# Optimization experiments

Measured on AMD Instinct MI355X. Metric: run time of the kernel, lower is better.

The kernel has to match this reference:

```python
import jax, jax.numpy as jnp
import numpy as np

N = 50000
E = 800000
IN_FEAT = 256
HIDDEN = 256
NUM_CLASS = 10
NUM_GRAPHS = 512
LAYERS = 2


def setup_inputs() -> dict:
    key = jax.random.key(0)
    ks = jax.random.split(key, 10)
    x = jax.random.normal(ks[0], (N, IN_FEAT), dtype=jnp.float32)
    edge_index = jax.random.randint(ks[1], (2, E), 0, N, dtype=jnp.int32)
    batch = jnp.sort(jax.random.randint(ks[2], (N,), 0, NUM_GRAPHS, dtype=jnp.int32))
    s_in = 1.0 / np.sqrt(IN_FEAT)
    s_h = 1.0 / np.sqrt(HIDDEN)
    enc_W = jax.random.uniform(ks[3], (IN_FEAT, HIDDEN), jnp.float32, -s_in, s_in)
    enc_b = jax.random.uniform(ks[4], (HIDDEN,), jnp.float32, -s_in, s_in)
    conv_W = jax.random.uniform(ks[5], (LAYERS, HIDDEN, HIDDEN), jnp.float32, -s_h, s_h)
    conv_b = jax.random.uniform(ks[6], (LAYERS, HIDDEN), jnp.float32, -s_h, s_h)
    out_W = jax.random.uniform(ks[7], (HIDDEN, NUM_CLASS), jnp.float32, -s_h, s_h)
    out_b = jax.random.uniform(ks[8], (NUM_CLASS,), jnp.float32, -s_h, s_h)
    return {"x": x, "edge_index": edge_index, "batch": batch,
            "enc_W": enc_W, "enc_b": enc_b,
            "conv_W": conv_W, "conv_b": conv_b,
            "out_W": out_W, "out_b": out_b}


def _gcn_conv(x, row, col, deg_norm_edge, W, b):
    # PyG GCNConv: linear transform, then normalized scatter-add aggregation.
    h = x @ W                                   # [N, H]
    msg = h[row] * deg_norm_edge[:, None]       # [E+N, H] gather + scale
    out = jax.ops.segment_sum(msg, col, num_segments=N)  # scatter-add
    return out + b


def reference(x, edge_index, batch, enc_W, enc_b, conv_W, conv_b, out_W, out_b):
    # self-loops appended once (same structure every layer)
    loops = jnp.arange(N, dtype=edge_index.dtype)
    row = jnp.concatenate([edge_index[0], loops])  # source
    col = jnp.concatenate([edge_index[1], loops])  # target
    deg = jax.ops.segment_sum(jnp.ones_like(col, dtype=x.dtype), col, num_segments=N)
    dinv = jnp.where(deg > 0, jax.lax.rsqrt(deg), 0.0)
    norm = dinv[row] * dinv[col]                # symmetric GCN normalization per edge

    h = x @ enc_W + enc_b
    for i in range(LAYERS):
        h = jax.nn.relu(_gcn_conv(h, row, col, norm, conv_W[i], conv_b[i]))

    # global_mean_pool over `batch` segment ids
    sums = jax.ops.segment_sum(h, batch, num_segments=NUM_GRAPHS)
    cnts = jax.ops.segment_sum(jnp.ones((N,), dtype=h.dtype), batch, num_segments=NUM_GRAPHS)
    pooled = sums / jnp.maximum(cnts, 1.0)[:, None]

    # dropout is identity in eval mode
    return pooled @ out_W + out_b
```

## Files before the change

kernel.cpp:

```cpp
#include <hip/hip_runtime.h>

#define NN 50000
#define NE 800000
#define HD 256
#define NG 512
#define NC 10
#define GEMM_G ((NN + 31) / 32)
#define NP 196
#define HB 200
#define CHUNK (NE / HB)
#define NODES_PER_HB (NN / HB)

typedef unsigned short u16;
typedef unsigned char u8;
typedef short v8s __attribute__((ext_vector_type(8)));
typedef float v4f __attribute__((ext_vector_type(4)));
typedef float v2f __attribute__((ext_vector_type(2)));
typedef u16 v4u __attribute__((ext_vector_type(4)));
typedef u16 v8u __attribute__((ext_vector_type(8)));

static __device__ __forceinline__ float bf2f(u16 u) {
    return __uint_as_float(((unsigned)u) << 16);
}
static __device__ __forceinline__ u16 f2bf(float f) {
    unsigned u = __float_as_uint(f);
    unsigned r = (u + 0x7fffu + ((u >> 16) & 1u)) >> 16;
    return (u16)r;
}
static __device__ __forceinline__ int clampi(int v, int lo, int hi) {
    return min(max(v, lo), hi);
}
static __device__ __forceinline__ float ldf(const void* p, size_t i, int isbf) {
    return isbf ? bf2f(((const u16*)p)[i]) : ((const float*)p)[i];
}

static __device__ __forceinline__ u8 f32_to_fp8(float f) {
#if __has_builtin(__builtin_amdgcn_cvt_pk_fp8_f32)
    int r = __builtin_amdgcn_cvt_pk_fp8_f32(f, f, 0, false);
    return (u8)(r & 0xff);
#else
    float a = fabsf(f);
    unsigned s = (__float_as_uint(f) >> 31) << 7;
    if (a < 0.0009765625f) return (u8)s;
    a = fminf(a, 448.f);
    if (a < 0.015625f) {
        int m = (int)(a * 512.f + 0.5f);
        return (u8)(s | min(m, 7));
    }
    unsigned u = __float_as_uint(a);
    unsigned r = u + 0x0007FFFFu + ((u >> 20) & 1u);
    int e = (int)(r >> 23) - 127 + 7;
    if (e > 15) return (u8)(s | 0x7E);
    unsigned m = (r >> 20) & 7u;
    return (u8)(s | ((unsigned)e << 3) | m);
#endif
}
static __device__ __forceinline__ v4f fp8x4_to_f32(unsigned v) {
#if __has_builtin(__builtin_amdgcn_cvt_pk_f32_fp8)
    v2f lo = __builtin_amdgcn_cvt_pk_f32_fp8(v, false);
    v2f hi = __builtin_amdgcn_cvt_pk_f32_fp8(v, true);
    return (v4f){lo[0], lo[1], hi[0], hi[1]};
#else
    v4f o;
#pragma unroll
    for (int j = 0; j < 4; j++) {
        unsigned b = (v >> (8 * j)) & 0xffu;
        unsigned e = (b >> 3) & 15u, m = b & 7u;
        float val = e ? __uint_as_float(((e + 120u) << 23) | (m << 20))
                      : (float)m * 0.001953125f;
        o[j] = (b & 0x80u) ? -val : val;
    }
    return o;
#endif
}

__global__ void k_detect(const u16* __restrict__ xu, int* __restrict__ mode) {
    __shared__ int cnt;
    if (threadIdx.x == 0) cnt = 0;
    __syncthreads();
    int bad = 0;
    for (int i = threadIdx.x; i < 4096; i += 256) {
        float v = bf2f(xu[2 * i]);
        float av = fabsf(v);
        if (av > 100.f || (av < 1e-3f && av != 0.f)) bad++;
    }
    atomicAdd(&cnt, bad);
    __syncthreads();
    if (threadIdx.x == 0) mode[0] = (cnt > 1024) ? 0 : 1;
}

__global__ void k_prep(const void* __restrict__ enc_W, const void* __restrict__ conv_W,
                       const void* __restrict__ enc_b, const void* __restrict__ conv_b,
                       const void* __restrict__ out_b,
                       u16* __restrict__ Wp, float* __restrict__ biasf,
                       const int* __restrict__ modep) {
    int md = modep[0];
    int b = blockIdx.x;
    if (b < 768) {
        int wi = b >> 8;
        int n = b & 255, k = threadIdx.x;
        const void* W = (wi == 0) ? enc_W : conv_W;
        size_t off = (wi == 0) ? 0 : (size_t)(wi - 1) * HD * HD;
        int nt = n >> 4, m = n & 15;
        int ks = k >> 5, q = (k >> 3) & 3, j = k & 7;
        size_t idx = ((((size_t)nt * 8 + ks) * 64) + q * 16 + m) * 8 + j;
        Wp[(size_t)wi * HD * HD + idx] = f2bf(ldf(W, off + (size_t)k * HD + n, md));
    } else {
        for (int j = threadIdx.x; j < 768 + NC; j += 256) {
            float v = (j < 256) ? ldf(enc_b, j, md)
                    : (j < 768) ? ldf(conv_b, j - 256, md)
                                : ldf(out_b, j - 768, md);
            biasf[j] = v;
        }
    }
}

static __device__ __forceinline__ void hist_body(
        int b, const int* __restrict__ ecol, const int* __restrict__ batch,
        int* __restrict__ bh, int* __restrict__ gptr, int* hist) {
    int tid = threadIdx.x;
    if (tid < NP) hist[tid] = 0;
    __syncthreads();
    int e0 = b * CHUNK;
    for (int i = tid; i < CHUNK; i += 256) {
        int c = clampi(ecol[e0 + i], 0, NN - 1);
        atomicAdd(&hist[c >> 8], 1);
    }
    int n0 = b * NODES_PER_HB;
    for (int i = tid; i < NODES_PER_HB; i += 256) {
        int idx = n0 + i;
        int bb = clampi(batch[idx], 0, NG - 1);
        int bp = (idx == 0) ? -1 : clampi(batch[idx - 1], 0, NG - 1);
        for (int g = bp + 1; g <= bb; g++) gptr[g] = idx;
        if (idx == NN - 1)
            for (int g = bb + 1; g <= NG; g++) gptr[g] = NN;
    }
    __syncthreads();
    if (tid < NP) bh[(size_t)tid * HB + b] = hist[tid];
}

static __device__ __forceinline__ void scat_body(
        int b, const int* __restrict__ erow, const int* __restrict__ ecol,
        const int* __restrict__ pptr, const int* __restrict__ base,
        unsigned* __restrict__ pairbuf, int* lfill) {
    int tid = threadIdx.x;
    if (tid < NP) lfill[tid] = 0;
    __syncthreads();
    int e0 = b * CHUNK;
    for (int i = tid; i < CHUNK; i += 256) {
        int c = clampi(ecol[e0 + i], 0, NN - 1);
        int rw = clampi(erow[e0 + i], 0, NN - 1);
        int p = c >> 8;
        int r = atomicAdd(&lfill[p], 1);
        int pos = pptr[p] + base[(size_t)p * HB + b] + r;
        pairbuf[pos] = ((unsigned)rw << 8) | (unsigned)(c & 255);
    }
}

static __device__ __forceinline__ void gemm_body(
        int bid, u16* As, const void* __restrict__ A, const u16* __restrict__ Wp,
        const float* __restrict__ biasf, void* __restrict__ out,
        int M, int hasBias, int outFp8, int amode) {
    int tid = threadIdx.x;
    int wave = tid >> 6;
    int lane = tid & 63;
    int row0 = bid * 32;
    if (row0 >= M) return;
    int m = lane & 15, q = lane >> 4;

#pragma unroll
    for (int it = 0; it < 4; it++) {
        int fb = it * 4 + wave;
        int mt = fb >> 3, ks = fb & 7;
        int row = min(row0 + mt * 16 + m, M - 1);
        int colE = ks * 32 + q * 8;
        v8s v;
        if (amode) {
            v = *(const v8s*)((const u16*)A + (size_t)row * HD + colE);
        } else {
            const float* af = (const float*)A + (size_t)row * HD + colE;
            v4f x0 = *(const v4f*)af;
            v4f x1 = *(const v4f*)(af + 4);
            v[0] = (short)f2bf(x0[0]); v[1] = (short)f2bf(x0[1]);
            v[2] = (short)f2bf(x0[2]); v[3] = (short)f2bf(x0[3]);
            v[4] = (short)f2bf(x1[0]); v[5] = (short)f2bf(x1[1]);
            v[6] = (short)f2bf(x1[2]); v[7] = (short)f2bf(x1[3]);
        }
        *(v8s*)&As[((size_t)fb * 64 + lane) * 8] = v;
    }
    __syncthreads();

    v4f acc[2][4];
#pragma unroll
    for (int i = 0; i < 2; i++)
#pragma unroll
        for (int j = 0; j < 4; j++) acc[i][j] = (v4f){0.f, 0.f, 0.f, 0.f};

    const u16* wp = Wp + (size_t)wave * 4 * 8 * 64 * 8;

#pragma unroll
    for (int ks = 0; ks < 8; ks++) {
        v8s bfr[4];
#pragma unroll
        for (int nt = 0; nt < 4; nt++)
            bfr[nt] = *(const v8s*)(wp + ((size_t)(nt * 8 + ks) * 64 + lane) * 8);
        v8s a[2];
#pragma unroll
        for (int mt = 0; mt < 2; mt++)
            a[mt] = *(const v8s*)&As[((size_t)(mt * 8 + ks) * 64 + lane) * 8];
#pragma unroll
        for (int mt = 0; mt < 2; mt++)
#pragma unroll
            for (int nt = 0; nt < 4; nt++)
                acc[mt][nt] = __builtin_amdgcn_mfma_f32_16x16x32_bf16(
                    a[mt], bfr[nt], acc[mt][nt], 0, 0, 0);
    }
    if (outFp8) {
#pragma unroll
        for (int mt = 0; mt < 2; mt++) {
#pragma unroll
            for (int nt = 0; nt < 4; nt++) {
                int ocol = wave * 64 + nt * 16 + m;
#pragma unroll
                for (int r = 0; r < 4; r++) {
                    int orow = row0 + mt * 16 + q * 4 + r;
                    if (orow < M)
                        ((u8*)out)[(size_t)orow * HD + ocol] =
                            f32_to_fp8(acc[mt][nt][r] * 32.f);
                }
            }
        }
    } else {
#pragma unroll
        for (int mt = 0; mt < 2; mt++) {
#pragma unroll
            for (int nt = 0; nt < 4; nt++) {
                int ocol = wave * 64 + nt * 16 + m;
                float badd = hasBias ? biasf[ocol] : 0.f;
#pragma unroll
                for (int r = 0; r < 4; r++) {
                    int orow = row0 + mt * 16 + q * 4 + r;
                    if (orow < M)
                        ((u16*)out)[(size_t)orow * HD + ocol] =
                            f2bf(acc[mt][nt][r] + badd);
                }
            }
        }
    }
}

static __device__ __forceinline__ void agg_node(
        const u8* __restrict__ t, const int* __restrict__ cptr,
        const int* __restrict__ csrc, const float* __restrict__ dinv,
        const float* __restrict__ biasf, int node, int lane, float* o) {
    int half = lane >> 5;
    int f0 = (lane & 31) * 8;
    const u8* tf = t + f0;
    float dn = dinv[node];
    float a[8];
#pragma unroll
    for (int k = 0; k < 8; k++) a[k] = 0.f;

    if (half == 0) {
        uint2 sv = *(const uint2*)(tf + (size_t)node * HD);
        v4f lo = fp8x4_to_f32(sv.x), hi = fp8x4_to_f32(sv.y);
#pragma unroll
        for (int k = 0; k < 4; k++) {
            a[k] += lo[k] * dn;
            a[k + 4] += hi[k] * dn;
        }
    }

    int e0 = cptr[node], e1 = cptr[node + 1];
    e1 = clampi(e1, 0, NE);
    e0 = clampi(e0, 0, e1);
    int e = e0;
    for (; e + 16 <= e1; e += 16) {
        int s[8];
#pragma unroll
        for (int j = 0; j < 8; j++)
            s[j] = clampi(csrc[e + 2 * j + half], 0, NN - 1);
        uint2 rv[8];
        float wv[8];
#pragma unroll
        for (int j = 0; j < 8; j++) {
            rv[j] = *(const uint2*)(tf + (size_t)s[j] * HD);
            wv[j] = dinv[s[j]];
        }
#pragma unroll
        for (int j = 0; j < 8; j++) {
            v4f lo = fp8x4_to_f32(rv[j].x), hi = fp8x4_to_f32(rv[j].y);
#pragma unroll
            for (int k = 0; k < 4; k++) {
                a[k] = fmaf(lo[k], wv[j], a[k]);
                a[k + 4] = fmaf(hi[k], wv[j], a[k + 4]);
            }
        }
    }
    for (; e + 2 <= e1; e += 2) {
        int s = clampi(csrc[e + half], 0, NN - 1);
        uint2 rv = *(const uint2*)(tf + (size_t)s * HD);
        float wv = dinv[s];
        v4f lo = fp8x4_to_f32(rv.x), hi = fp8x4_to_f32(rv.y);
#pragma unroll
        for (int k = 0; k < 4; k++) {
            a[k] = fmaf(lo[k], wv, a[k]);
            a[k + 4] = fmaf(hi[k], wv, a[k + 4]);
        }
    }
    if (e < e1 && half == 0) {
        int s = clampi(csrc[e], 0, NN - 1);
        uint2 rv = *(const uint2*)(tf + (size_t)s * HD);
        float wv = dinv[s];
        v4f lo = fp8x4_to_f32(rv.x), hi = fp8x4_to_f32(rv.y);
#pragma unroll
        for (int k = 0; k < 4; k++) {
            a[k] = fmaf(lo[k], wv, a[k]);
            a[k + 4] = fmaf(hi[k], wv, a[k + 4]);
        }
    }
#pragma unroll
    for (int k = 0; k < 8; k++) a[k] += __shfl_xor(a[k], 32, 64);

    float sc = dn * 0.03125f;
    v4f b0 = *(const v4f*)(biasf + f0);
    v4f b1 = *(const v4f*)(biasf + f0 + 4);
#pragma unroll
    for (int k = 0; k < 4; k++) {
        o[k] = fmaxf(fmaf(a[k], sc, b0[k]), 0.f);
        o[k + 4] = fmaxf(fmaf(a[k + 4], sc, b1[k]), 0.f);
    }
}

__global__ __launch_bounds__(256) void k_gemm(
        const void* __restrict__ A, const u16* __restrict__ Wp,
        const float* __restrict__ biasf, void* __restrict__ out,
        int M, int hasBias, int outFp8,
        const int* __restrict__ modep, int forceBf) {
    __shared__ u16 As[16 * 64 * 8];
    gemm_body(blockIdx.x, As, A, Wp, biasf, out, M, hasBias, outFp8,
              forceBf ? 1 : modep[0]);
}

__global__ __launch_bounds__(256) void k_hist(
        const int* __restrict__ ecol, const int* __restrict__ batch,
        int* __restrict__ bh, int* __restrict__ gptr) {
    __shared__ int hist[NP];
    hist_body(blockIdx.x, ecol, batch, bh, gptr, hist);
}

__global__ __launch_bounds__(256) void k_scat(
        const int* __restrict__ erow, const int* __restrict__ ecol,
        const int* __restrict__ pptr, const int* __restrict__ base,
        unsigned* __restrict__ pairbuf) {
    __shared__ int lfill[NP];
    scat_body(blockIdx.x, erow, ecol, pptr, base, pairbuf, lfill);
}

__global__ __launch_bounds__(256) void k_gemm_hist(
        const void* __restrict__ A, const u16* __restrict__ Wp,
        const float* __restrict__ biasf, void* __restrict__ out,
        int M, int hasBias, const int* __restrict__ modep, int forceBf,
        const int* __restrict__ ecol, const int* __restrict__ batch,
        int* __restrict__ bh, int* __restrict__ gptr) {
    __shared__ u16 As[16 * 64 * 8];
    __shared__ int hist[NP];
    if (blockIdx.x < HB) {
        hist_body(blockIdx.x, ecol, batch, bh, gptr, hist);
    } else {
        gemm_body(blockIdx.x - HB, As, A, Wp, biasf, out, M, hasBias, 0,
                  forceBf ? 1 : modep[0]);
    }
}

__global__ __launch_bounds__(256) void k_scat_gemm1(
        const void* __restrict__ A, const u16* __restrict__ Wp,
        void* __restrict__ out, int M,
        const int* __restrict__ erow, const int* __restrict__ ecol,
        const int* __restrict__ pptr, const int* __restrict__ base,
        unsigned* __restrict__ pairbuf) {
    __shared__ u16 As[16 * 64 * 8];
    __shared__ int lfill[NP];
    if (blockIdx.x < HB) {
        scat_body(blockIdx.x, erow, ecol, pptr, base, pairbuf, lfill);
    } else {
        gemm_body(blockIdx.x - HB, As, A, Wp, nullptr, out, M, 0, 1, 1);
    }
}

__global__ __launch_bounds__(256) void k_aggregate2(
        const u8* __restrict__ t, const int* __restrict__ cptr,
        const int* __restrict__ csrc, const float* __restrict__ dinv,
        const float* __restrict__ biasf, u16* __restrict__ out) {
    int wave = threadIdx.x >> 6, lane = threadIdx.x & 63;
    int node = blockIdx.x * 4 + wave;
    if (node >= NN) return;
    float o[8];
    agg_node(t, cptr, csrc, dinv, biasf, node, lane, o);
    if (lane < 32) {
        v8u pk;
#pragma unroll
        for (int k = 0; k < 8; k++) pk[k] = f2bf(o[k]);
        *(v8u*)(out + (size_t)node * HD + lane * 8) = pk;
    }
}

__global__ __launch_bounds__(256) void k_scanA(
        const int* __restrict__ bh, int* __restrict__ base, int* __restrict__ ptot) {
    int p = blockIdx.x, t = threadIdx.x;
    int v = (t < HB) ? bh[(size_t)p * HB + t] : 0;
    __shared__ int sh[256];
    sh[t] = v;
    __syncthreads();
    for (int off = 1; off < 256; off <<= 1) {
        int x = (t >= off) ? sh[t - off] : 0;
        __syncthreads();
        sh[t] += x;
        __syncthreads();
    }
    if (t < HB) base[(size_t)p * HB + t] = sh[t] - v;
    if (t == 0) ptot[p] = sh[255];
}

__global__ __launch_bounds__(256) void k_scanB(
        const int* __restrict__ ptot, int* __restrict__ pptr) {
    int t = threadIdx.x;
    int v = (t < NP) ? ptot[t] : 0;
    __shared__ int sh[256];
    sh[t] = v;
    __syncthreads();
    for (int off = 1; off < 256; off <<= 1) {
        int x = (t >= off) ? sh[t - off] : 0;
        __syncthreads();
        sh[t] += x;
        __syncthreads();
    }
    if (t < NP) pptr[t] = sh[t] - v;
    if (t == 0) pptr[NP] = sh[255];
}

__global__ __launch_bounds__(256) void k_part2(
        const int* __restrict__ pptr, const unsigned* __restrict__ pairbuf,
        int* __restrict__ cptr, float* __restrict__ dinv, int* __restrict__ csrc) {
    int p = blockIdx.x, t = threadIdx.x;
    int seg0 = pptr[p], seg1 = pptr[p + 1];
    __shared__ int hist[256], sums[256], fill[256];
    hist[t] = 0;
    fill[t] = 0;
    __syncthreads();
    for (int i = seg0 + t; i < seg1; i += 256)
        atomicAdd(&hist[pairbuf[i] & 255], 1);
    __syncthreads();
    int d = hist[t];
    sums[t] = d;
    __syncthreads();
    for (int off = 1; off < 256; off <<= 1) {
        int x = (t >= off) ? sums[t - off] : 0;
        __syncthreads();
        sums[t] += x;
        __syncthreads();
    }
    int ex = sums[t] - d;
    int c = p * 256 + t;
    if (c < NN) {
        cptr[c] = seg0 + ex;
        dinv[c] = rsqrtf((float)(d + 1));
    }
    if (p == NP - 1 && t == 0) cptr[NN] = NE;
    __syncthreads();
    sums[t] = ex;
    __syncthreads();
    for (int i = seg0 + t; i < seg1; i += 256) {
        unsigned v = pairbuf[i];
        int cl = v & 255;
        int r = atomicAdd(&fill[cl], 1);
        csrc[seg0 + sums[cl] + r] = (int)(v >> 8);
    }
}

__global__ __launch_bounds__(256) void k_head(
        const u16* __restrict__ h, const int* __restrict__ gptr,
        const void* __restrict__ W, const float* __restrict__ biasf,
        void* __restrict__ outv, const int* __restrict__ modep) {
    int md = modep[0];
    int g = blockIdx.x, f = threadIdx.x;
    int hi = clampi(gptr[g + 1], 0, NN);
    int lo = clampi(gptr[g], 0, hi);
    float s0 = 0.f, s1 = 0.f, s2 = 0.f, s3 = 0.f;
    int i = lo;
    for (; i + 4 <= hi; i += 4) {
        s0 += bf2f(h[(size_t)i * HD + f]);
        s1 += bf2f(h[(size_t)(i + 1) * HD + f]);
        s2 += bf2f(h[(size_t)(i + 2) * HD + f]);
        s3 += bf2f(h[(size_t)(i + 3) * HD + f]);
    }
    for (; i < hi; i++) s0 += bf2f(h[(size_t)i * HD + f]);
    __shared__ float ps[256];
    ps[f] = ((s0 + s1) + (s2 + s3)) / fmaxf((float)(hi - lo), 1.0f);
    __syncthreads();
    if (threadIdx.x < 64) {
        int lane = threadIdx.x;
        float acc[NC];
#pragma unroll
        for (int c = 0; c < NC; c++) acc[c] = 0.f;
        for (int k = lane; k < HD; k += 64) {
            float p = ps[k];
#pragma unroll
            for (int c = 0; c < NC; c++) acc[c] += p * ldf(W, (size_t)k * NC + c, md);
        }
#pragma unroll
        for (int c = 0; c < NC; c++) {
            for (int off = 32; off > 0; off >>= 1)
                acc[c] += __shfl_down(acc[c], off, 64);
        }
        if (lane == 0) {
#pragma unroll
            for (int c = 0; c < NC; c++) {
                float vv = acc[c] + biasf[768 + c];
                if (md) ((u16*)outv)[g * NC + c] = f2bf(vv);
                else    ((float*)outv)[g * NC + c] = vv;
            }
        }
    }
}

extern "C" void kernel_launch(void* const* d_in, const int* in_sizes, int n_in,
                              void* d_out, int out_size, void* d_ws, size_t ws_size,
                              hipStream_t stream) {
    const void* x      = d_in[0];
    const int*  ei     = (const int*)d_in[1];
    const int*  batch  = (const int*)d_in[2];
    const void* enc_W  = d_in[3];
    const void* enc_b  = d_in[4];
    const void* conv_W = d_in[5];
    const void* conv_b = d_in[6];
    const void* out_W  = d_in[7];
    const void* out_b  = d_in[8];

    char* w = (char*)d_ws;
    auto alloc = [&](size_t b) { char* p = w; w += (b + 255) & ~(size_t)255; return p; };
    int*   mode   = (int*)alloc(256);
    float* dinv   = (float*)alloc(NN * 4);
    int*   cptr   = (int*)alloc((NN + 1) * 4);
    int*   gptr   = (int*)alloc((NG + 1) * 4);
    int*   csrc   = (int*)alloc((size_t)NE * 4);
    u16*   Wp     = (u16*)alloc((size_t)3 * HD * HD * 2);
    float* biasf  = (float*)alloc(778 * 4);
    u16*   hbuf   = (u16*)alloc((size_t)NN * HD * 2);
    size_t scratch_need = ((size_t)2 * NP * HB + 2 * NP + 1) * 4 + (size_t)NE * 4 + 1024;
    size_t used = (size_t)(w - (char*)d_ws);
    bool fused = (used + scratch_need <= ws_size);
    char* sb = fused ? alloc(scratch_need) : (char*)hbuf;
    int* bh   = (int*)sb;
    int* base = bh + (size_t)NP * HB;
    int* ptot = base + (size_t)NP * HB;
    int* pptr = ptot + NP;
    unsigned* pairbuf = (unsigned*)(pptr + NP + 1);
    u8* tbuf = (u8*)d_in[0];

    const int* erow = ei;
    const int* ecol = ei + NE;

    k_detect<<<1, 256, 0, stream>>>((const u16*)x, mode);
    k_prep<<<769, 256, 0, stream>>>(enc_W, conv_W, enc_b, conv_b, out_b, Wp, biasf, mode);

    if (fused) {
        k_gemm_hist<<<HB + GEMM_G, 256, 0, stream>>>(
            x, Wp, biasf, hbuf, NN, 1, mode, 0, ecol, batch, bh, gptr);
        k_scanA<<<NP, 256, 0, stream>>>(bh, base, ptot);
        k_scanB<<<1, 256, 0, stream>>>(ptot, pptr);
        k_scat_gemm1<<<HB + GEMM_G, 256, 0, stream>>>(
            hbuf, Wp + (size_t)HD * HD, tbuf, NN, erow, ecol, pptr, base, pairbuf);
        k_part2<<<NP, 256, 0, stream>>>(pptr, pairbuf, cptr, dinv, csrc);
    } else {
        k_hist<<<HB, 256, 0, stream>>>(ecol, batch, bh, gptr);
        k_scanA<<<NP, 256, 0, stream>>>(bh, base, ptot);
        k_scanB<<<1, 256, 0, stream>>>(ptot, pptr);
        k_scat<<<HB, 256, 0, stream>>>(erow, ecol, pptr, base, pairbuf);
        k_part2<<<NP, 256, 0, stream>>>(pptr, pairbuf, cptr, dinv, csrc);
        k_gemm<<<GEMM_G, 256, 0, stream>>>(x, Wp, biasf, hbuf, NN, 1, 0, mode, 0);
        k_gemm<<<GEMM_G, 256, 0, stream>>>(hbuf, Wp + (size_t)HD * HD, nullptr,
                                           tbuf, NN, 0, 1, mode, 1);
    }
    k_aggregate2<<<(NN + 3) / 4, 256, 0, stream>>>(tbuf, cptr, csrc, dinv,
                                                   biasf + 256, hbuf);
    k_gemm<<<GEMM_G, 256, 0, stream>>>(hbuf, Wp + (size_t)2 * HD * HD, nullptr,
                                       tbuf, NN, 0, 1, mode, 1);
    k_aggregate2<<<(NN + 3) / 4, 256, 0, stream>>>(tbuf, cptr, csrc, dinv,
                                                   biasf + 256 + HD, hbuf);
    k_head<<<NG, 256, 0, stream>>>(hbuf, gptr, out_W, biasf, d_out, mode);
}
```

Before: 287.6 us.

## Make GEMM persistent with 8 waves and register-resident weight fragments

The GEMM blocks now use 512 threads (8 waves), each wave owning 32 output columns, and preload their full weight fragments into registers once. A fixed grid of 521 blocks loops over the 32-row tiles, so weights are loaded once per block instead of once per tile. The fused hist/scatter bodies take a thread-count parameter so they work with 512-thread blocks. The trade-off is higher register pressure, which may lower occupancy, and an extra barrier per tile iteration.

```diff
diff --git a/kernel.cpp b/kernel.cpp
--- a/kernel.cpp
+++ b/kernel.cpp
@@ -5,7 +5,8 @@
 #define HD 256
 #define NG 512
 #define NC 10
-#define GEMM_G ((NN + 31) / 32)
+#define TILES ((NN + 31) / 32)
+#define GEMM_G 521
 #define NP 196
 #define HB 200
 #define CHUNK (NE / HB)
@@ -116,18 +117,19 @@
 }
 
 static __device__ __forceinline__ void hist_body(
-        int b, const int* __restrict__ ecol, const int* __restrict__ batch,
+        int b, int nthreads, const int* __restrict__ ecol,
+        const int* __restrict__ batch,
         int* __restrict__ bh, int* __restrict__ gptr, int* hist) {
     int tid = threadIdx.x;
     if (tid < NP) hist[tid] = 0;
     __syncthreads();
     int e0 = b * CHUNK;
-    for (int i = tid; i < CHUNK; i += 256) {
+    for (int i = tid; i < CHUNK; i += nthreads) {
         int c = clampi(ecol[e0 + i], 0, NN - 1);
         atomicAdd(&hist[c >> 8], 1);
     }
     int n0 = b * NODES_PER_HB;
-    for (int i = tid; i < NODES_PER_HB; i += 256) {
+    for (int i = tid; i < NODES_PER_HB; i += nthreads) {
         int idx = n0 + i;
         int bb = clampi(batch[idx], 0, NG - 1);
         int bp = (idx == 0) ? -1 : clampi(batch[idx - 1], 0, NG - 1);
@@ -140,14 +142,15 @@
 }
 
 static __device__ __forceinline__ void scat_body(
-        int b, const int* __restrict__ erow, const int* __restrict__ ecol,
+        int b, int nthreads, const int* __restrict__ erow,
+        const int* __restrict__ ecol,
         const int* __restrict__ pptr, const int* __restrict__ base,
         unsigned* __restrict__ pairbuf, int* lfill) {
     int tid = threadIdx.x;
     if (tid < NP) lfill[tid] = 0;
     __syncthreads();
     int e0 = b * CHUNK;
-    for (int i = tid; i < CHUNK; i += 256) {
+    for (int i = tid; i < CHUNK; i += nthreads) {
         int c = clampi(ecol[e0 + i], 0, NN - 1);
         int rw = clampi(erow[e0 + i], 0, NN - 1);
         int p = c >> 8;
@@ -157,95 +160,99 @@
     }
 }
 
-static __device__ __forceinline__ void gemm_body(
-        int bid, u16* As, const void* __restrict__ A, const u16* __restrict__ Wp,
+static __device__ __forceinline__ void gemm_body8(
+        int gb, u16* As, const void* __restrict__ A, const u16* __restrict__ Wp,
         const float* __restrict__ biasf, void* __restrict__ out,
         int M, int hasBias, int outFp8, int amode) {
     int tid = threadIdx.x;
     int wave = tid >> 6;
     int lane = tid & 63;
-    int row0 = bid * 32;
-    if (row0 >= M) return;
     int m = lane & 15, q = lane >> 4;
 
-#pragma unroll
-    for (int it = 0; it < 4; it++) {
-        int fb = it * 4 + wave;
-        int mt = fb >> 3, ks = fb & 7;
-        int row = min(row0 + mt * 16 + m, M - 1);
-        int colE = ks * 32 + q * 8;
-        v8s v;
-        if (amode) {
-            v = *(const v8s*)((const u16*)A + (size_t)row * HD + colE);
-        } else {
-            const float* af = (const float*)A + (size_t)row * HD + colE;
-            v4f x0 = *(const v4f*)af;
-            v4f x1 = *(const v4f*)(af + 4);
-            v[0] = (short)f2bf(x0[0]); v[1] = (short)f2bf(x0[1]);
-            v[2] = (short)f2bf(x0[2]); v[3] = (short)f2bf(x0[3]);
-            v[4] = (short)f2bf(x1[0]); v[5] = (short)f2bf(x1[1]);
-            v[6] = (short)f2bf(x1[2]); v[7] = (short)f2bf(x1[3]);
-        }
-        *(v8s*)&As[((size_t)fb * 64 + lane) * 8] = v;
-    }
-    __syncthreads();
-
-    v4f acc[2][4];
-#pragma unroll
-    for (int i = 0; i < 2; i++)
-#pragma unroll
-        for (int j = 0; j < 4; j++) acc[i][j] = (v4f){0.f, 0.f, 0.f, 0.f};
-
-    const u16* wp = Wp + (size_t)wave * 4 * 8 * 64 * 8;
-
-#pragma unroll
-    for (int ks = 0; ks < 8; ks++) {
-        v8s bfr[4];
-#pragma unroll
-        for (int nt = 0; nt < 4; nt++)
-            bfr[nt] = *(const v8s*)(wp + ((size_t)(nt * 8 + ks) * 64 + lane) * 8);
-        v8s a[2];
-#pragma unroll
-        for (int mt = 0; mt < 2; mt++)
-            a[mt] = *(const v8s*)&As[((size_t)(mt * 8 + ks) * 64 + lane) * 8];
-#pragma unroll
-        for (int mt = 0; mt < 2; mt++)
-#pragma unroll
-            for (int nt = 0; nt < 4; nt++)
-                acc[mt][nt] = __builtin_amdgcn_mfma_f32_16x16x32_bf16(
-                    a[mt], bfr[nt], acc[mt][nt], 0, 0, 0);
-    }
-    if (outFp8) {
-#pragma unroll
-        for (int mt = 0; mt < 2; mt++) {
-#pragma unroll
-            for (int nt = 0; nt < 4; nt++) {
-                int ocol = wave * 64 + nt * 16 + m;
-#pragma unroll
-                for (int r = 0; r < 4; r++) {
-                    int orow = row0 + mt * 16 + q * 4 + r;
-                    if (orow < M)
-                        ((u8*)out)[(size_t)orow * HD + ocol] =
-                            f32_to_fp8(acc[mt][nt][r] * 32.f);
+    v8s bf[2][8];
+#pragma unroll
+    for (int nt = 0; nt < 2; nt++)
+#pragma unroll
+        for (int ks = 0; ks < 8; ks++)
+            bf[nt][ks] = *(const v8s*)(Wp +
+                ((size_t)((wave * 2 + nt) * 8 + ks) * 64 + lane) * 8);
+
+    for (int tile = gb; tile < TILES; tile += GEMM_G) {
+        int row0 = tile * 32;
+#pragma unroll
+        for (int it = 0; it < 2; it++) {
+            int fb = it * 8 + wave;
+            int mt = fb >> 3, ks = fb & 7;
+            int row = min(row0 + mt * 16 + m, M - 1);
+            int colE = ks * 32 + q * 8;
+            v8s v;
+            if (amode) {
+                v = *(const v8s*)((const u16*)A + (size_t)row * HD + colE);
+            } else {
+                const float* af = (const float*)A + (size_t)row * HD + colE;
+                v4f x0 = *(const v4f*)af;
+                v4f x1 = *(const v4f*)(af + 4);
+                v[0] = (short)f2bf(x0[0]); v[1] = (short)f2bf(x0[1]);
+                v[2] = (short)f2bf(x0[2]); v[3] = (short)f2bf(x0[3]);
+                v[4] = (short)f2bf(x1[0]); v[5] = (short)f2bf(x1[1]);
+                v[6] = (short)f2bf(x1[2]); v[7] = (short)f2bf(x1[3]);
+            }
+            *(v8s*)&As[((size_t)fb * 64 + lane) * 8] = v;
+        }
+        __syncthreads();
+
+        v4f acc[2][2];
+#pragma unroll
+        for (int i = 0; i < 2; i++)
+#pragma unroll
+            for (int j = 0; j < 2; j++) acc[i][j] = (v4f){0.f, 0.f, 0.f, 0.f};
+
+#pragma unroll
+        for (int ks = 0; ks < 8; ks++) {
+            v8s a0 = *(const v8s*)&As[((size_t)ks * 64 + lane) * 8];
+            v8s a1 = *(const v8s*)&As[((size_t)(8 + ks) * 64 + lane) * 8];
+            acc[0][0] = __builtin_amdgcn_mfma_f32_16x16x32_bf16(
+                a0, bf[0][ks], acc[0][0], 0, 0, 0);
+            acc[0][1] = __builtin_amdgcn_mfma_f32_16x16x32_bf16(
+                a0, bf[1][ks], acc[0][1], 0, 0, 0);
+            acc[1][0] = __builtin_amdgcn_mfma_f32_16x16x32_bf16(
+                a1, bf[0][ks], acc[1][0], 0, 0, 0);
+            acc[1][1] = __builtin_amdgcn_mfma_f32_16x16x32_bf16(
+                a1, bf[1][ks], acc[1][1], 0, 0, 0);
+        }
+        if (outFp8) {
+#pragma unroll
+            for (int mt = 0; mt < 2; mt++) {
+#pragma unroll
+                for (int nt = 0; nt < 2; nt++) {
+                    int ocol = wave * 32 + nt * 16 + m;
+#pragma unroll
+                    for (int r = 0; r < 4; r++) {
+                        int orow = row0 + mt * 16 + q * 4 + r;
+                        if (orow < M)
+                            ((u8*)out)[(size_t)orow * HD + ocol] =
+                                f32_to_fp8(acc[mt][nt][r] * 32.f);
+                    }
                 }
             }
-        }
-    } else {
-#pragma unroll
-        for (int mt = 0; mt < 2; mt++) {
-#pragma unroll
-            for (int nt = 0; nt < 4; nt++) {
-                int ocol = wave * 64 + nt * 16 + m;
-                float badd = hasBias ? biasf[ocol] : 0.f;
-#pragma unroll
-                for (int r = 0; r < 4; r++) {
-                    int orow = row0 + mt * 16 + q * 4 + r;
-                    if (orow < M)
-                        ((u16*)out)[(size_t)orow * HD + ocol] =
-                            f2bf(acc[mt][nt][r] + badd);
+        } else {
+#pragma unroll
+            for (int mt = 0; mt < 2; mt++) {
+#pragma unroll
+                for (int nt = 0; nt < 2; nt++) {
+                    int ocol = wave * 32 + nt * 16 + m;
+                    float badd = hasBias ? biasf[ocol] : 0.f;
+#pragma unroll
+                    for (int r = 0; r < 4; r++) {
+                        int orow = row0 + mt * 16 + q * 4 + r;
+                        if (orow < M)
+                            ((u16*)out)[(size_t)orow * HD + ocol] =
+                                f2bf(acc[mt][nt][r] + badd);
+                    }
                 }
             }
         }
+        __syncthreads();
     }
 }
 
@@ -332,21 +339,21 @@
     }
 }
 
-__global__ __launch_bounds__(256) void k_gemm(
+__global__ __launch_bounds__(512) void k_gemm(
         const void* __restrict__ A, const u16* __restrict__ Wp,
         const float* __restrict__ biasf, void* __restrict__ out,
         int M, int hasBias, int outFp8,
         const int* __restrict__ modep, int forceBf) {
     __shared__ u16 As[16 * 64 * 8];
-    gemm_body(blockIdx.x, As, A, Wp, biasf, out, M, hasBias, outFp8,
-              forceBf ? 1 : modep[0]);
+    gemm_body8(blockIdx.x, As, A, Wp, biasf, out, M, hasBias, outFp8,
+               forceBf ? 1 : modep[0]);
 }
 
 __global__ __launch_bounds__(256) void k_hist(
         const int* __restrict__ ecol, const int* __restrict__ batch,
         int* __restrict__ bh, int* __restrict__ gptr) {
     __shared__ int hist[NP];
-    hist_body(blockIdx.x, ecol, batch, bh, gptr, hist);
+    hist_body(blockIdx.x, 256, ecol, batch, bh, gptr, hist);
 }
 
 __global__ __launch_bounds__(256) void k_scat(
@@ -354,10 +361,10 @@
         const int* __restrict__ pptr, const int* __restrict__ base,
         unsigned* __restrict__ pairbuf) {
     __shared__ int lfill[NP];
-    scat_body(blockIdx.x, erow, ecol, pptr, base, pairbuf, lfill);
-}
-
-__global__ __launch_bounds__(256) void k_gemm_hist(
+    scat_body(blockIdx.x, 256, erow, ecol, pptr, base, pairbuf, lfill);
+}
+
+__global__ __launch_bounds__(512) void k_gemm_hist(
         const void* __restrict__ A, const u16* __restrict__ Wp,
         const float* __restrict__ biasf, void* __restrict__ out,
         int M, int hasBias, const int* __restrict__ modep, int forceBf,
@@ -366,14 +373,14 @@
     __shared__ u16 As[16 * 64 * 8];
     __shared__ int hist[NP];
     if (blockIdx.x < HB) {
-        hist_body(blockIdx.x, ecol, batch, bh, gptr, hist);
+        hist_body(blockIdx.x, 512, ecol, batch, bh, gptr, hist);
     } else {
-        gemm_body(blockIdx.x - HB, As, A, Wp, biasf, out, M, hasBias, 0,
-                  forceBf ? 1 : modep[0]);
-    }
-}
-
-__global__ __launch_bounds__(256) void k_scat_gemm1(
+        gemm_body8(blockIdx.x - HB, As, A, Wp, biasf, out, M, hasBias, 0,
+                   forceBf ? 1 : modep[0]);
+    }
+}
+
+__global__ __launch_bounds__(512) void k_scat_gemm1(
         const void* __restrict__ A, const u16* __restrict__ Wp,
         void* __restrict__ out, int M,
         const int* __restrict__ erow, const int* __restrict__ ecol,
@@ -382,9 +389,9 @@
     __shared__ u16 As[16 * 64 * 8];
     __shared__ int lfill[NP];
     if (blockIdx.x < HB) {
-        scat_body(blockIdx.x, erow, ecol, pptr, base, pairbuf, lfill);
+        scat_body(blockIdx.x, 512, erow, ecol, pptr, base, pairbuf, lfill);
     } else {
-        gemm_body(blockIdx.x - HB, As, A, Wp, nullptr, out, M, 0, 1, 1);
+        gemm_body8(blockIdx.x - HB, As, A, Wp, nullptr, out, M, 0, 1, 1);
     }
 }
 
@@ -565,11 +572,11 @@
     k_prep<<<769, 256, 0, stream>>>(enc_W, conv_W, enc_b, conv_b, out_b, Wp, biasf, mode);
 
     if (fused) {
-        k_gemm_hist<<<HB + GEMM_G, 256, 0, stream>>>(
+        k_gemm_hist<<<HB + GEMM_G, 512, 0, stream>>>(
             x, Wp, biasf, hbuf, NN, 1, mode, 0, ecol, batch, bh, gptr);
         k_scanA<<<NP, 256, 0, stream>>>(bh, base, ptot);
         k_scanB<<<1, 256, 0, stream>>>(ptot, pptr);
-        k_scat_gemm1<<<HB + GEMM_G, 256, 0, stream>>>(
+        k_scat_gemm1<<<HB + GEMM_G, 512, 0, stream>>>(
             hbuf, Wp + (size_t)HD * HD, tbuf, NN, erow, ecol, pptr, base, pairbuf);
         k_part2<<<NP, 256, 0, stream>>>(pptr, pairbuf, cptr, dinv, csrc);
     } else {
@@ -578,13 +585,13 @@
         k_scanB<<<1, 256, 0, stream>>>(ptot, pptr);
         k_scat<<<HB, 256, 0, stream>>>(erow, ecol, pptr, base, pairbuf);
         k_part2<<<NP, 256, 0, stream>>>(pptr, pairbuf, cptr, dinv, csrc);
-        k_gemm<<<GEMM_G, 256, 0, stream>>>(x, Wp, biasf, hbuf, NN, 1, 0, mode, 0);
-        k_gemm<<<GEMM_G, 256, 0, stream>>>(hbuf, Wp + (size_t)HD * HD, nullptr,
+        k_gemm<<<GEMM_G, 512, 0, stream>>>(x, Wp, biasf, hbuf, NN, 1, 0, mode, 0);
+        k_gemm<<<GEMM_G, 512, 0, stream>>>(hbuf, Wp + (size_t)HD * HD, nullptr,
                                            tbuf, NN, 0, 1, mode, 1);
     }
     k_aggregate2<<<(NN + 3) / 4, 256, 0, stream>>>(tbuf, cptr, csrc, dinv,
                                                    biasf + 256, hbuf);
-    k_gemm<<<GEMM_G, 256, 0, stream>>>(hbuf, Wp + (size_t)2 * HD * HD, nullptr,
+    k_gemm<<<GEMM_G, 512, 0, stream>>>(hbuf, Wp + (size_t)2 * HD * HD, nullptr,
                                        tbuf, NN, 0, 1, mode, 1);
     k_aggregate2<<<(NN + 3) / 4, 256, 0, stream>>>(tbuf, cptr, csrc, dinv,
                                                    biasf + 256 + HD, hbuf);
```

New measurement: 289.4 us. About the same (+0.6%).

## Use direct global-to-LDS loads with XOR-swizzled A tile and fold detect into prep

Applied to the files above, without the earlier changes.

The GEMM A-tile staging switches to a row-major, XOR-swizzled LDS layout. For bf16 inputs it is filled with global_load_lds (direct global-to-LDS DMA), which skips the register round trip. The MFMA A-fragment reads index the swizzled layout so they avoid bank conflicts. The separate k_detect launch is folded into every k_prep block, removing one launch but repeating the 4096-element scan in each of 769 blocks. Kernel definitions are moved after the gemm body and GEMM_G is renamed to TILES.

```diff
diff --git a/kernel.cpp b/kernel.cpp
--- a/kernel.cpp
+++ b/kernel.cpp
@@ -5,7 +5,7 @@
 #define HD 256
 #define NG 512
 #define NC 10
-#define GEMM_G ((NN + 31) / 32)
+#define TILES ((NN + 31) / 32)
 #define NP 196
 #define HB 200
 #define CHUNK (NE / HB)
@@ -74,9 +74,19 @@
 #endif
 }
 
-__global__ void k_detect(const u16* __restrict__ xu, int* __restrict__ mode) {
-    __shared__ int cnt;
-    if (threadIdx.x == 0) cnt = 0;
+static __device__ __forceinline__ void gload_lds16(const void* g, void* l) {
+#if __has_builtin(__builtin_amdgcn_global_load_lds)
+    __builtin_amdgcn_global_load_lds(
+        (const __attribute__((address_space(1))) void*)g,
+        (__attribute__((address_space(3))) void*)l, 16, 0, 0);
+#else
+    *(v8s*)(l) = *(const v8s*)(g);
+#endif
+}
+
+static __device__ __forceinline__ int detect_mode_block(
+        const u16* __restrict__ xu, int* sh) {
+    if (threadIdx.x == 0) sh[0] = 0;
     __syncthreads();
     int bad = 0;
     for (int i = threadIdx.x; i < 4096; i += 256) {
@@ -84,17 +94,19 @@
         float av = fabsf(v);
         if (av > 100.f || (av < 1e-3f && av != 0.f)) bad++;
     }
-    atomicAdd(&cnt, bad);
-    __syncthreads();
-    if (threadIdx.x == 0) mode[0] = (cnt > 1024) ? 0 : 1;
-}
-
-__global__ void k_prep(const void* __restrict__ enc_W, const void* __restrict__ conv_W,
+    atomicAdd(sh, bad);
+    __syncthreads();
+    return (sh[0] > 1024) ? 0 : 1;
+}
+
+__global__ void k_prep(const u16* __restrict__ xu,
+                       const void* __restrict__ enc_W, const void* __restrict__ conv_W,
                        const void* __restrict__ enc_b, const void* __restrict__ conv_b,
                        const void* __restrict__ out_b,
                        u16* __restrict__ Wp, float* __restrict__ biasf,
-                       const int* __restrict__ modep) {
-    int md = modep[0];
+                       int* __restrict__ modep) {
+    __shared__ int sh[1];
+    int md = detect_mode_block(xu, sh);
     int b = blockIdx.x;
     if (b < 768) {
         int wi = b >> 8;
@@ -112,6 +124,7 @@
                                 : ldf(out_b, j - 768, md);
             biasf[j] = v;
         }
+        if (threadIdx.x == 0) modep[0] = md;
     }
 }
 
@@ -168,25 +181,46 @@
     if (row0 >= M) return;
     int m = lane & 15, q = lane >> 4;
 
-#pragma unroll
-    for (int it = 0; it < 4; it++) {
-        int fb = it * 4 + wave;
-        int mt = fb >> 3, ks = fb & 7;
-        int row = min(row0 + mt * 16 + m, M - 1);
-        int colE = ks * 32 + q * 8;
-        v8s v;
-        if (amode) {
-            v = *(const v8s*)((const u16*)A + (size_t)row * HD + colE);
-        } else {
-            const float* af = (const float*)A + (size_t)row * HD + colE;
+    if (amode) {
+#if __has_builtin(__builtin_amdgcn_global_load_lds)
+#pragma unroll
+        for (int j = 0; j < 4; j++) {
+            int slot = j * 256 + tid;
+            int row = slot >> 5, sb = slot & 31;
+            int gb = sb ^ (row & 7);
+            const u16* src = (const u16*)A +
+                (size_t)min(row0 + row, M - 1) * HD + gb * 8;
+            u16* dst = As + ((size_t)j * 256 + wave * 64) * 8;
+            gload_lds16(src, dst);
+        }
+#else
+#pragma unroll
+        for (int j = 0; j < 4; j++) {
+            int slot = j * 256 + tid;
+            int row = slot >> 5, sb = slot & 31;
+            int gb = sb ^ (row & 7);
+            const u16* src = (const u16*)A +
+                (size_t)min(row0 + row, M - 1) * HD + gb * 8;
+            *(v8s*)&As[(size_t)slot * 8] = *(const v8s*)src;
+        }
+#endif
+    } else {
+#pragma unroll
+        for (int j = 0; j < 4; j++) {
+            int slot = j * 256 + tid;
+            int row = slot >> 5, sb = slot & 31;
+            int gb = sb ^ (row & 7);
+            const float* af = (const float*)A +
+                (size_t)min(row0 + row, M - 1) * HD + gb * 8;
             v4f x0 = *(const v4f*)af;
             v4f x1 = *(const v4f*)(af + 4);
+            v8s v;
             v[0] = (short)f2bf(x0[0]); v[1] = (short)f2bf(x0[1]);
             v[2] = (short)f2bf(x0[2]); v[3] = (short)f2bf(x0[3]);
             v[4] = (short)f2bf(x1[0]); v[5] = (short)f2bf(x1[1]);
             v[6] = (short)f2bf(x1[2]); v[7] = (short)f2bf(x1[3]);
-        }
-        *(v8s*)&As[((size_t)fb * 64 + lane) * 8] = v;
+            *(v8s*)&As[(size_t)slot * 8] = v;
+        }
     }
     __syncthreads();
 
@@ -206,8 +240,11 @@
             bfr[nt] = *(const v8s*)(wp + ((size_t)(nt * 8 + ks) * 64 + lane) * 8);
         v8s a[2];
 #pragma unroll
-        for (int mt = 0; mt < 2; mt++)
-            a[mt] = *(const v8s*)&As[((size_t)(mt * 8 + ks) * 64 + lane) * 8];
+        for (int mt = 0; mt < 2; mt++) {
+            int row = mt * 16 + m;
+            a[mt] = *(const v8s*)&As[(size_t)row * 256 +
+                                     (size_t)(((ks * 4 + q) ^ (m & 7)) * 8)];
+        }
 #pragma unroll
         for (int mt = 0; mt < 2; mt++)
 #pragma unroll
@@ -246,6 +283,62 @@
                 }
             }
         }
+    }
+}
+
+__global__ __launch_bounds__(256) void k_gemm(
+        const void* __restrict__ A, const u16* __restrict__ Wp,
+        const float* __restrict__ biasf, void* __restrict__ out,
+        int M, int hasBias, int outFp8,
+        const int* __restrict__ modep, int forceBf) {
+    __shared__ u16 As[32 * 256];
+    gemm_body(blockIdx.x, As, A, Wp, biasf, out, M, hasBias, outFp8,
+              forceBf ? 1 : modep[0]);
+}
+
+__global__ __launch_bounds__(256) void k_hist(
+        const int* __restrict__ ecol, const int* __restrict__ batch,
+        int* __restrict__ bh, int* __restrict__ gptr) {
+    __shared__ int hist[NP];
+    hist_body(blockIdx.x, ecol, batch, bh, gptr, hist);
+}
+
+__global__ __launch_bounds__(256) void k_scat(
+        const int* __restrict__ erow, const int* __restrict__ ecol,
+        const int* __restrict__ pptr, const int* __restrict__ base,
+        unsigned* __restrict__ pairbuf) {
+    __shared__ int lfill[NP];
+    scat_body(blockIdx.x, erow, ecol, pptr, base, pairbuf, lfill);
+}
+
+__global__ __launch_bounds__(256) void k_gemm_hist(
+        const void* __restrict__ A, const u16* __restrict__ Wp,
+        const float* __restrict__ biasf, void* __restrict__ out,
+        int M, int hasBias, const int* __restrict__ modep, int forceBf,
+        const int* __restrict__ ecol, const int* __restrict__ batch,
+        int* __restrict__ bh, int* __restrict__ gptr) {
+    __shared__ u16 As[32 * 256];
+    __shared__ int hist[NP];
+    if (blockIdx.x < HB) {
+        hist_body(blockIdx.x, ecol, batch, bh, gptr, hist);
+    } else {
+        gemm_body(blockIdx.x - HB, As, A, Wp, biasf, out, M, hasBias, 0,
+                  forceBf ? 1 : modep[0]);
+    }
+}
+
+__global__ __launch_bounds__(256) void k_scat_gemm1(
+        const void* __restrict__ A, const u16* __restrict__ Wp,
+        void* __restrict__ out, int M,
+        const int* __restrict__ erow, const int* __restrict__ ecol,
+        const int* __restrict__ pptr, const int* __restrict__ base,
+        unsigned* __restrict__ pairbuf) {
+    __shared__ u16 As[32 * 256];
+    __shared__ int lfill[NP];
+    if (blockIdx.x < HB) {
+        scat_body(blockIdx.x, erow, ecol, pptr, base, pairbuf, lfill);
+    } else {
+        gemm_body(blockIdx.x - HB, As, A, Wp, nullptr, out, M, 0, 1, 1);
     }
 }
 
@@ -329,62 +422,6 @@
     for (int k = 0; k < 4; k++) {
         o[k] = fmaxf(fmaf(a[k], sc, b0[k]), 0.f);
         o[k + 4] = fmaxf(fmaf(a[k + 4], sc, b1[k]), 0.f);
-    }
-}
-
-__global__ __launch_bounds__(256) void k_gemm(
-        const void* __restrict__ A, const u16* __restrict__ Wp,
-        const float* __restrict__ biasf, void* __restrict__ out,
-        int M, int hasBias, int outFp8,
-        const int* __restrict__ modep, int forceBf) {
-    __shared__ u16 As[16 * 64 * 8];
-    gemm_body(blockIdx.x, As, A, Wp, biasf, out, M, hasBias, outFp8,
-              forceBf ? 1 : modep[0]);
-}
-
-__global__ __launch_bounds__(256) void k_hist(
-        const int* __restrict__ ecol, const int* __restrict__ batch,
-        int* __restrict__ bh, int* __restrict__ gptr) {
-    __shared__ int hist[NP];
-    hist_body(blockIdx.x, ecol, batch, bh, gptr, hist);
-}
-
-__global__ __launch_bounds__(256) void k_scat(
-        const int* __restrict__ erow, const int* __restrict__ ecol,
-        const int* __restrict__ pptr, const int* __restrict__ base,
-        unsigned* __restrict__ pairbuf) {
-    __shared__ int lfill[NP];
-    scat_body(blockIdx.x, erow, ecol, pptr, base, pairbuf, lfill);
-}
-
-__global__ __launch_bounds__(256) void k_gemm_hist(
-        const void* __restrict__ A, const u16* __restrict__ Wp,
-        const float* __restrict__ biasf, void* __restrict__ out,
-        int M, int hasBias, const int* __restrict__ modep, int forceBf,
-        const int* __restrict__ ecol, const int* __restrict__ batch,
-        int* __restrict__ bh, int* __restrict__ gptr) {
-    __shared__ u16 As[16 * 64 * 8];
-    __shared__ int hist[NP];
-    if (blockIdx.x < HB) {
-        hist_body(blockIdx.x, ecol, batch, bh, gptr, hist);
-    } else {
-        gemm_body(blockIdx.x - HB, As, A, Wp, biasf, out, M, hasBias, 0,
-                  forceBf ? 1 : modep[0]);
-    }
-}
-
-__global__ __launch_bounds__(256) void k_scat_gemm1(
-        const void* __restrict__ A, const u16* __restrict__ Wp,
-        void* __restrict__ out, int M,
-        const int* __restrict__ erow, const int* __restrict__ ecol,
-        const int* __restrict__ pptr, const int* __restrict__ base,
-        unsigned* __restrict__ pairbuf) {
-    __shared__ u16 As[16 * 64 * 8];
-    __shared__ int lfill[NP];
-    if (blockIdx.x < HB) {
-        scat_body(blockIdx.x, erow, ecol, pptr, base, pairbuf, lfill);
-    } else {
-        gemm_body(blockIdx.x - HB, As, A, Wp, nullptr, out, M, 0, 1, 1);
     }
 }
 
@@ -561,15 +598,15 @@
     const int* erow = ei;
     const int* ecol = ei + NE;
 
-    k_detect<<<1, 256, 0, stream>>>((const u16*)x, mode);
-    k_prep<<<769, 256, 0, stream>>>(enc_W, conv_W, enc_b, conv_b, out_b, Wp, biasf, mode);
+    k_prep<<<769, 256, 0, stream>>>((const u16*)x, enc_W, conv_W, enc_b,
+                                    conv_b, out_b, Wp, biasf, mode);
 
     if (fused) {
-        k_gemm_hist<<<HB + GEMM_G, 256, 0, stream>>>(
+        k_gemm_hist<<<HB + TILES, 256, 0, stream>>>(
             x, Wp, biasf, hbuf, NN, 1, mode, 0, ecol, batch, bh, gptr);
         k_scanA<<<NP, 256, 0, stream>>>(bh, base, ptot);
         k_scanB<<<1, 256, 0, stream>>>(ptot, pptr);
-        k_scat_gemm1<<<HB + GEMM_G, 256, 0, stream>>>(
+        k_scat_gemm1<<<HB + TILES, 256, 0, stream>>>(
             hbuf, Wp + (size_t)HD * HD, tbuf, NN, erow, ecol, pptr, base, pairbuf);
         k_part2<<<NP, 256, 0, stream>>>(pptr, pairbuf, cptr, dinv, csrc);
     } else {
@@ -578,14 +615,14 @@
         k_scanB<<<1, 256, 0, stream>>>(ptot, pptr);
         k_scat<<<HB, 256, 0, stream>>>(erow, ecol, pptr, base, pairbuf);
         k_part2<<<NP, 256, 0, stream>>>(pptr, pairbuf, cptr, dinv, csrc);
-        k_gemm<<<GEMM_G, 256, 0, stream>>>(x, Wp, biasf, hbuf, NN, 1, 0, mode, 0);
-        k_gemm<<<GEMM_G, 256, 0, stream>>>(hbuf, Wp + (size_t)HD * HD, nullptr,
-                                           tbuf, NN, 0, 1, mode, 1);
+        k_gemm<<<TILES, 256, 0, stream>>>(x, Wp, biasf, hbuf, NN, 1, 0, mode, 0);
+        k_gemm<<<TILES, 256, 0, stream>>>(hbuf, Wp + (size_t)HD * HD, nullptr,
+                                          tbuf, NN, 0, 1, mode, 1);
     }
     k_aggregate2<<<(NN + 3) / 4, 256, 0, stream>>>(tbuf, cptr, csrc, dinv,
                                                    biasf + 256, hbuf);
-    k_gemm<<<GEMM_G, 256, 0, stream>>>(hbuf, Wp + (size_t)2 * HD * HD, nullptr,
-                                       tbuf, NN, 0, 1, mode, 1);
+    k_gemm<<<TILES, 256, 0, stream>>>(hbuf, Wp + (size_t)2 * HD * HD, nullptr,
+                                      tbuf, NN, 0, 1, mode, 1);
     k_aggregate2<<<(NN + 3) / 4, 256, 0, stream>>>(tbuf, cptr, csrc, dinv,
                                                    biasf + 256 + HD, hbuf);
     k_head<<<NG, 256, 0, stream>>>(hbuf, gptr, out_W, biasf, d_out, mode);
```

Result: no change. 283.6 us (-1.4%).
